# Kernel tuning notes

Measured on AMD Instinct MI355X. Metric: run time of the kernel, lower is better.

## Reference

```python
import jax, jax.numpy as jnp
import numpy as np

MAX_TOP_K = 64          # max(top_k) across the batch, as in sample_from_logit dispatch
NEG_INF = -1e30
B, V, T = 256, 128000, 16


def setup_inputs() -> dict:
    key = jax.random.key(0)
    k1, k2, k3, k4, k5, k6 = jax.random.split(key, 6)
    logits = jax.random.normal(k1, (B, V), dtype=jnp.float32)
    temperature = jax.random.uniform(k2, (B,), dtype=jnp.float32) + 0.5   # (0.5, 1.5)
    top_k = jax.random.randint(k3, (B,), 1, MAX_TOP_K, dtype=jnp.int32)
    top_p = jax.random.uniform(k4, (B,), dtype=jnp.float32)               # (0, 1)
    min_p = jax.random.uniform(k5, (B,), dtype=jnp.float32) * 0.1         # small min-p
    target_ids = jax.random.randint(k6, (B, T), 0, V, dtype=jnp.int32)
    return {"logits": logits, "temperature": temperature, "top_k": top_k,
            "top_p": top_p, "min_p": min_p, "target_ids": target_ids}


def _sample_from_logit(logits, temperature, top_k, top_p, min_p):
    # temperature scaling
    temp = jnp.maximum(temperature, 0.05)
    scaled = logits / temp[:, None]                    # [B, V]
    # restrict to the max_top_k candidates once (sorted descending)
    vals, idx = jax.lax.top_k(scaled, MAX_TOP_K)       # [B, K], [B, K]
    pos = jnp.arange(MAX_TOP_K)[None, :]
    k = jnp.clip(top_k, 1, MAX_TOP_K)
    keep_k = pos < k[:, None]                          # per-request top-k mask
    vals = jnp.where(keep_k, vals, NEG_INF)
    probs = jax.nn.softmax(vals, axis=-1)              # renormalized over kept set
    # top-p (nucleus): keep tokens whose preceding cumulative mass < top_p
    csum = jnp.cumsum(probs, axis=-1)
    keep_p = (csum - probs) < top_p[:, None]
    # min-p: keep tokens with prob >= min_p * max_prob (max is column 0, sorted desc)
    keep_m = probs >= min_p[:, None] * probs[:, :1]
    keep = (keep_k & keep_p & keep_m).at[:, 0].set(True)  # always keep the argmax
    filt_logp = jnp.where(keep, jnp.log(probs + 1e-20), NEG_INF)
    # multinomial sample via Gumbel-max (renormalization is implicit)
    g = jax.random.gumbel(jax.random.key(42), filt_logp.shape, dtype=filt_logp.dtype)
    choice = jnp.argmax(filt_logp + g, axis=-1)        # [B] index into top-K set
    return jnp.take_along_axis(idx, choice[:, None], axis=1)[:, 0]  # vocab ids


def reference(logits, temperature, top_k, top_p, min_p, target_ids):
    next_token_ids = _sample_from_logit(logits, temperature, top_k, top_p, min_p)  # [B]
    # perplexity gather: ppls = -log_softmax(logits); ppl[i, j] = ppls[i, target_ids[i, j]]
    logZ = jax.nn.logsumexp(logits, axis=-1, keepdims=True)          # [B, 1]
    tgt_logits = jnp.take_along_axis(logits, target_ids, axis=1)     # [B, T]
    ppl = -(tgt_logits - logZ)                                       # [B, T]
    return next_token_ids, ppl
```

## Files before the change

### kernel.cpp

```cpp
#include <hip/hip_runtime.h>
#include <stdint.h>

#define B_ 256
#define V_ 128000
#define T_ 16
#define K_ 64
#define NEG_INF_ (-1e30f)

#define CAP   4096
#define NT    1024

__device__ __forceinline__ uint32_t rotl32(uint32_t x, uint32_t d) {
  return (x << d) | (x >> (32u - d));
}

__device__ uint32_t threefry_bits_partitionable(uint32_t f) {
  const uint32_t ks0 = 0u;
  const uint32_t ks1 = 42u;
  const uint32_t ks2 = 0x1BD11BDAu ^ 0u ^ 42u;
  uint32_t x0 = 0u;
  uint32_t x1 = f;
  x0 += ks0; x1 += ks1;
#define R4(a,b,c,d) \
  x0 += x1; x1 = rotl32(x1,a); x1 ^= x0; \
  x0 += x1; x1 = rotl32(x1,b); x1 ^= x0; \
  x0 += x1; x1 = rotl32(x1,c); x1 ^= x0; \
  x0 += x1; x1 = rotl32(x1,d); x1 ^= x0;
  R4(13u,15u,26u,6u)   x0 += ks1; x1 += ks2 + 1u;
  R4(17u,29u,16u,24u)  x0 += ks2; x1 += ks0 + 2u;
  R4(13u,15u,26u,6u)   x0 += ks0; x1 += ks1 + 3u;
  R4(17u,29u,16u,24u)  x0 += ks1; x1 += ks2 + 4u;
  R4(13u,15u,26u,6u)   x0 += ks2; x1 += ks0 + 5u;
#undef R4
  return x0 ^ x1;
}

__global__ __launch_bounds__(NT) void sampler_kernel(
    const float* __restrict__ logits,
    const float* __restrict__ temperature,
    const int*   __restrict__ top_k,
    const float* __restrict__ top_p,
    const float* __restrict__ min_p,
    const int*   __restrict__ target_ids,
    float*       __restrict__ out)
{
  const int r   = blockIdx.x;
  const int tid = threadIdx.x;
  const float* __restrict__ row = logits + (size_t)r * V_;

  __shared__ unsigned long long s_cand[CAP];
  __shared__ unsigned int       s_candcount;
  __shared__ float              s_wavesum[NT / 64];
  __shared__ unsigned long long s_top[K_];
  __shared__ float              s_g[K_];
  __shared__ float              s_logZ;
  __shared__ int                s_ncand;

  if (tid < K_) s_top[tid] = 0ull;
  if (tid == 0) s_candcount = 0u;
  __syncthreads();

  const float temp = fmaxf(temperature[r], 0.05f);

  float a0 = 0.0f, a1 = 0.0f, a2 = 0.0f, a3 = 0.0f;
  const float4* row4 = reinterpret_cast<const float4*>(row);
  const int nf4 = V_ / 4;

#define PROC4(vv, i4) do {                                                     \
    a0 += __expf(vv.x); a1 += __expf(vv.y);                                    \
    a2 += __expf(vv.z); a3 += __expf(vv.w);                                    \
    float mx_ = fmaxf(fmaxf(vv.x, vv.y), fmaxf(vv.z, vv.w));                   \
    if (mx_ > 3.0f) {                                                          \
      float xs_[4] = {vv.x, vv.y, vv.z, vv.w};                                 \
      _Pragma("unroll")                                                        \
      for (int c_ = 0; c_ < 4; ++c_) {                                         \
        if (xs_[c_] > 3.0f) {                                                  \
          unsigned int slot_ = atomicAdd(&s_candcount, 1u);                    \
          if (slot_ < CAP) {                                                   \
            float scaled_ = xs_[c_] / temp;                                    \
            uint32_t idx_ = (uint32_t)((i4) * 4 + c_);                         \
            s_cand[slot_] =                                                    \
              ((unsigned long long)__float_as_uint(scaled_) << 32) |           \
              (unsigned long long)(0xFFFFFFFFu - idx_);                        \
          }                                                                    \
        }                                                                      \
      }                                                                        \
    }                                                                          \
  } while (0)

  int base = 0;
  for (; base + NT * 4 <= nf4; base += NT * 4) {
    const int i0 = base + tid, i1 = i0 + NT, i2 = i1 + NT, i3 = i2 + NT;
    float4 v0 = row4[i0];
    float4 v1 = row4[i1];
    float4 v2 = row4[i2];
    float4 v3 = row4[i3];
    PROC4(v0, i0); PROC4(v1, i1); PROC4(v2, i2); PROC4(v3, i3);
  }
  for (int i = base + tid; i < nf4; i += NT) {
    float4 v = row4[i];
    PROC4(v, i);
  }
#undef PROC4

  float esum = (a0 + a1) + (a2 + a3);
  for (int off = 32; off > 0; off >>= 1) esum += __shfl_down(esum, off, 64);
  if ((tid & 63) == 0) s_wavesum[tid >> 6] = esum;
  __syncthreads();
  if (tid == 0) {
    float t = 0.0f;
    for (int w = 0; w < NT / 64; ++w) t += s_wavesum[w];
    s_logZ = logf(t);
    int nc = (int)s_candcount; if (nc > CAP) nc = CAP;
    s_ncand = nc;
  }
  __syncthreads();

  int ncand = s_ncand;
  for (int tier = 0; tier < 2 && ncand < K_; ++tier) {
    if (tid == 0) s_candcount = 0u;
    __syncthreads();
    const float thr = (tier == 0) ? 2.0f : -3.0e38f;
    for (int i = tid; i < V_; i += NT) {
      float x = row[i];
      if (x >= thr) {
        unsigned int slot = atomicAdd(&s_candcount, 1u);
        if (slot < CAP) {
          float scaled = x / temp;
          s_cand[slot] = ((unsigned long long)__float_as_uint(scaled) << 32) |
                         (unsigned long long)(0xFFFFFFFFu - (uint32_t)i);
        }
      }
    }
    __syncthreads();
    if (tid == 0) { int nc = (int)s_candcount; if (nc > CAP) nc = CAP; s_ncand = nc; }
    __syncthreads();
    ncand = s_ncand;
  }

  if (tid < K_) {
    uint32_t bits = threefry_bits_partitionable((uint32_t)(r * K_ + tid));
    float u01 = __uint_as_float((bits >> 9) | 0x3f800000u) - 1.0f;
    const float tiny = 1.1754943508222875e-38f;
    float u = fmaxf(tiny, u01 * (1.0f - tiny) + tiny);
    s_g[tid] = -logf(-logf(u));
  }

  if (tid < T_) {
    int tgt = target_ids[r * T_ + tid];
    out[B_ + r * T_ + tid] = s_logZ - row[tgt];
  }

  for (int c = tid; c < ncand; c += NT) {
    unsigned long long key = s_cand[c];
    int rank = 0;
    for (int j = 0; j < ncand; ++j) rank += (s_cand[j] > key) ? 1 : 0;
    if (rank < K_) s_top[rank] = key;
  }
  __syncthreads();

  if (tid == 0) {
    int kk = top_k[r];
    kk = kk < 1 ? 1 : (kk > K_ ? K_ : kk);
    const float tp = top_p[r], mp = min_p[r];
    const int nn = ncand < K_ ? ncand : K_;

    float e[K_];
    float m = 0.0f, sum = 0.0f;
    for (int i = 0; i < K_; ++i) {
      float v = (i < nn) ? __uint_as_float((uint32_t)(s_top[i] >> 32)) : NEG_INF_;
      if (i >= kk) v = NEG_INF_;
      if (i == 0) m = v;
      e[i] = expf(v - m);
      sum += e[i];
    }
    float csum = 0.0f, best = -INFINITY;
    int choice = 0;
    const float p0 = e[0] / sum;
    for (int i = 0; i < K_; ++i) {
      float pi = e[i] / sum;
      csum += pi;
      bool keep = (i < kk) && ((csum - pi) < tp) && (pi >= mp * p0);
      if (i == 0) keep = true;
      float fl = keep ? logf(pi + 1e-20f) : NEG_INF_;
      float sc = fl + s_g[i];
      if (sc > best) { best = sc; choice = i; }
    }
    int token = (int)(0xFFFFFFFFu - (uint32_t)(s_top[choice] & 0xFFFFFFFFull));
    out[r] = (float)token;
  }
}

extern "C" void kernel_launch(void* const* d_in, const int* in_sizes, int n_in,
                              void* d_out, int out_size, void* d_ws, size_t ws_size,
                              hipStream_t stream) {
  const float* logits      = (const float*)d_in[0];
  const float* temperature = (const float*)d_in[1];
  const int*   top_k       = (const int*)d_in[2];
  const float* top_p       = (const float*)d_in[3];
  const float* min_p       = (const float*)d_in[4];
  const int*   target_ids  = (const int*)d_in[5];
  float* out = (float*)d_out;
  (void)in_sizes; (void)n_in; (void)out_size; (void)d_ws; (void)ws_size;

  hipLaunchKernelGGL(sampler_kernel, dim3(B_), dim3(NT), 0, stream,
                     logits, temperature, top_k, top_p, min_p, target_ids, out);
}
```

Before: 41.38 us.

## Split each row across eight blocks with a global-candidate finalize kernel

The single 1024-thread block per row becomes a two-kernel pipeline. A streaming kernel gives each row to eight 256-thread blocks, which compute partial exp-sums and push candidates above 3.0 into a per-row global buffer using global atomics. A finalize kernel then ranks the candidates, computes logZ and the perplexity gather, and runs the sampling with the softmax steps parallelised over 64 threads. This aims for better occupancy and more bandwidth across the GPU. In exchange it adds a memset, a second launch and contended global atomics, and it falls back to the old kernel if the workspace is too small.

```diff
diff --git a/kernel.cpp b/kernel.cpp
--- a/kernel.cpp
+++ b/kernel.cpp
@@ -1,11 +1,19 @@
 #include <hip/hip_runtime.h>
 #include <stdint.h>
+
+typedef unsigned long long ull;
 
 #define B_ 256
 #define V_ 128000
 #define T_ 16
 #define K_ 64
 #define NEG_INF_ (-1e30f)
+
+#define PARTS   8
+#define NTA     256
+#define CHUNK4  (V_ / 4 / PARTS)
+#define CAPG    512
+#define CAPL    2048
 
 #define CAP   4096
 #define NT    1024
@@ -35,6 +43,198 @@
   return x0 ^ x1;
 }
 
+__global__ __launch_bounds__(NTA, 8) void stream_kernel(
+    const float* __restrict__ logits,
+    const float* __restrict__ temperature,
+    unsigned int* __restrict__ wcnt,
+    float*        __restrict__ wesum,
+    ull*          __restrict__ wcand)
+{
+  const int bid  = blockIdx.x;
+  const int r    = bid >> 3;
+  const int part = bid & 7;
+  const int tid  = threadIdx.x;
+
+  const float temp = fmaxf(temperature[r], 0.05f);
+  const float4* __restrict__ p4 =
+      reinterpret_cast<const float4*>(logits + (size_t)r * V_) + part * CHUNK4;
+  unsigned int* cntp = wcnt + r;
+  ull* candp = wcand + (size_t)r * CAPG;
+
+  float a0 = 0.0f, a1 = 0.0f, a2 = 0.0f, a3 = 0.0f;
+
+#define PROC4(vv, i4) do {                                                     \
+    a0 += __expf(vv.x); a1 += __expf(vv.y);                                    \
+    a2 += __expf(vv.z); a3 += __expf(vv.w);                                    \
+    float mx_ = fmaxf(fmaxf(vv.x, vv.y), fmaxf(vv.z, vv.w));                   \
+    if (mx_ > 3.0f) {                                                          \
+      float xs_[4] = {vv.x, vv.y, vv.z, vv.w};                                 \
+      _Pragma("unroll")                                                        \
+      for (int c_ = 0; c_ < 4; ++c_) {                                         \
+        if (xs_[c_] > 3.0f) {                                                  \
+          unsigned int slot_ = atomicAdd(cntp, 1u);                            \
+          if (slot_ < CAPG) {                                                  \
+            float scaled_ = xs_[c_] / temp;                                    \
+            uint32_t idx_ = (uint32_t)((part * CHUNK4 + (i4)) * 4 + c_);       \
+            candp[slot_] = ((ull)__float_as_uint(scaled_) << 32) |             \
+                           (ull)(0xFFFFFFFFu - idx_);                          \
+          }                                                                    \
+        }                                                                      \
+      }                                                                        \
+    }                                                                          \
+  } while (0)
+
+  int base = 0;
+  for (; base + NTA * 4 <= CHUNK4; base += NTA * 4) {
+    const int i0 = base + tid, i1 = i0 + NTA, i2 = i1 + NTA, i3 = i2 + NTA;
+    float4 v0 = p4[i0];
+    float4 v1 = p4[i1];
+    float4 v2 = p4[i2];
+    float4 v3 = p4[i3];
+    PROC4(v0, i0); PROC4(v1, i1); PROC4(v2, i2); PROC4(v3, i3);
+  }
+  for (int i = base + tid; i < CHUNK4; i += NTA) {
+    float4 v = p4[i];
+    PROC4(v, i);
+  }
+#undef PROC4
+
+  __shared__ float s_ws[NTA / 64];
+  float esum = (a0 + a1) + (a2 + a3);
+  for (int off = 32; off > 0; off >>= 1) esum += __shfl_down(esum, off, 64);
+  if ((tid & 63) == 0) s_ws[tid >> 6] = esum;
+  __syncthreads();
+  if (tid == 0) {
+    float t = 0.0f;
+    for (int w = 0; w < NTA / 64; ++w) t += s_ws[w];
+    wesum[bid] = t;
+  }
+}
+
+__global__ __launch_bounds__(256) void finalize_kernel(
+    const float* __restrict__ logits,
+    const float* __restrict__ temperature,
+    const int*   __restrict__ top_k,
+    const float* __restrict__ top_p,
+    const float* __restrict__ min_p,
+    const int*   __restrict__ target_ids,
+    const unsigned int* __restrict__ wcnt,
+    const float* __restrict__ wesum,
+    const ull*   __restrict__ wcand,
+    float*       __restrict__ out)
+{
+  const int r   = blockIdx.x;
+  const int tid = threadIdx.x;
+
+  __shared__ ull   s_cand[CAPL];
+  __shared__ ull   s_top[K_];
+  __shared__ float s_g[K_];
+  __shared__ float s_e[K_];
+  __shared__ float s_pi[K_];
+  __shared__ float s_lg[K_];
+  __shared__ float s_logZ, s_sum;
+  __shared__ unsigned int s_cc;
+
+  const float temp = fmaxf(temperature[r], 0.05f);
+
+  if (tid < K_) s_top[tid] = 0ull;
+
+  int cnt = (int)wcnt[r]; if (cnt > CAPG) cnt = CAPG;
+  for (int i = tid; i < cnt; i += 256) s_cand[i] = wcand[(size_t)r * CAPG + i];
+
+  if (tid == 0) {
+    float t = 0.0f;
+    for (int w = 0; w < PARTS; ++w) t += wesum[r * PARTS + w];
+    s_logZ = logf(t);
+  }
+  __syncthreads();
+
+  if (tid < T_) {
+    int tgt = target_ids[r * T_ + tid];
+    out[B_ + r * T_ + tid] = s_logZ - logits[(size_t)r * V_ + tgt];
+  }
+
+  int ncand = cnt;
+  for (int tier = 0; tier < 2 && ncand < K_; ++tier) {
+    __syncthreads();
+    if (tid == 0) s_cc = 0u;
+    __syncthreads();
+    const float thr = (tier == 0) ? 2.5f : -3.0e38f;
+    const float* rowp = logits + (size_t)r * V_;
+    for (int i = tid; i < V_; i += 256) {
+      float x = rowp[i];
+      if (x >= thr) {
+        unsigned int slot = atomicAdd(&s_cc, 1u);
+        if (slot < CAPL) {
+          float scaled = x / temp;
+          s_cand[slot] = ((ull)__float_as_uint(scaled) << 32) |
+                         (ull)(0xFFFFFFFFu - (uint32_t)i);
+        }
+      }
+    }
+    __syncthreads();
+    ncand = (int)(s_cc > CAPL ? CAPL : s_cc);
+  }
+
+  for (int c = tid; c < ncand; c += 256) {
+    ull key = s_cand[c];
+    int rank = 0;
+    for (int j = 0; j < ncand; ++j) rank += (s_cand[j] > key) ? 1 : 0;
+    if (rank < K_) s_top[rank] = key;
+  }
+  __syncthreads();
+
+  if (tid >= 64 && tid < 128) {
+    int i = tid - 64;
+    uint32_t bits = threefry_bits_partitionable((uint32_t)(r * K_ + i));
+    float u01 = __uint_as_float((bits >> 9) | 0x3f800000u) - 1.0f;
+    const float tiny = 1.1754943508222875e-38f;
+    float u = fmaxf(tiny, u01 * (1.0f - tiny) + tiny);
+    s_g[i] = -logf(-logf(u));
+  }
+
+  const int kk_raw = top_k[r];
+  const int kk = kk_raw < 1 ? 1 : (kk_raw > K_ ? K_ : kk_raw);
+  const int nn = ncand < K_ ? ncand : K_;
+
+  if (tid < K_) {
+    float v = (tid < nn) ? __uint_as_float((uint32_t)(s_top[tid] >> 32)) : NEG_INF_;
+    if (tid >= kk) v = NEG_INF_;
+    float v0 = (0 < nn) ? __uint_as_float((uint32_t)(s_top[0] >> 32)) : NEG_INF_;
+    s_e[tid] = expf(v - v0);
+  }
+  __syncthreads();
+  if (tid == 0) {
+    float sum = 0.0f;
+    for (int i = 0; i < K_; ++i) sum += s_e[i];
+    s_sum = sum;
+  }
+  __syncthreads();
+  if (tid < K_) {
+    float pi = s_e[tid] / s_sum;
+    s_pi[tid] = pi;
+    s_lg[tid] = logf(pi + 1e-20f);
+  }
+  __syncthreads();
+  if (tid == 0) {
+    const float tp = top_p[r], mp = min_p[r];
+    const float p0 = s_pi[0];
+    float csum = 0.0f, best = -INFINITY;
+    int choice = 0;
+    for (int i = 0; i < K_; ++i) {
+      float pi = s_pi[i];
+      csum += pi;
+      bool keep = (i < kk) && ((csum - pi) < tp) && (pi >= mp * p0);
+      if (i == 0) keep = true;
+      float fl = keep ? s_lg[i] : NEG_INF_;
+      float sc = fl + s_g[i];
+      if (sc > best) { best = sc; choice = i; }
+    }
+    int token = (int)(0xFFFFFFFFu - (uint32_t)(s_top[choice] & 0xFFFFFFFFull));
+    out[r] = (float)token;
+  }
+}
+
 __global__ __launch_bounds__(NT) void sampler_kernel(
     const float* __restrict__ logits,
     const float* __restrict__ temperature,
@@ -48,13 +248,13 @@
   const int tid = threadIdx.x;
   const float* __restrict__ row = logits + (size_t)r * V_;
 
-  __shared__ unsigned long long s_cand[CAP];
-  __shared__ unsigned int       s_candcount;
-  __shared__ float              s_wavesum[NT / 64];
-  __shared__ unsigned long long s_top[K_];
-  __shared__ float              s_g[K_];
-  __shared__ float              s_logZ;
-  __shared__ int                s_ncand;
+  __shared__ ull          s_cand[CAP];
+  __shared__ unsigned int s_candcount;
+  __shared__ float        s_wavesum[NT / 64];
+  __shared__ ull          s_top[K_];
+  __shared__ float        s_g[K_];
+  __shared__ float        s_logZ;
+  __shared__ int          s_ncand;
 
   if (tid < K_) s_top[tid] = 0ull;
   if (tid == 0) s_candcount = 0u;
@@ -79,9 +279,8 @@
           if (slot_ < CAP) {                                                   \
             float scaled_ = xs_[c_] / temp;                                    \
             uint32_t idx_ = (uint32_t)((i4) * 4 + c_);                         \
-            s_cand[slot_] =                                                    \
-              ((unsigned long long)__float_as_uint(scaled_) << 32) |           \
-              (unsigned long long)(0xFFFFFFFFu - idx_);                        \
+            s_cand[slot_] = ((ull)__float_as_uint(scaled_) << 32) |            \
+                            (ull)(0xFFFFFFFFu - idx_);                         \
           }                                                                    \
         }                                                                      \
       }                                                                        \
@@ -127,8 +326,8 @@
         unsigned int slot = atomicAdd(&s_candcount, 1u);
         if (slot < CAP) {
           float scaled = x / temp;
-          s_cand[slot] = ((unsigned long long)__float_as_uint(scaled) << 32) |
-                         (unsigned long long)(0xFFFFFFFFu - (uint32_t)i);
+          s_cand[slot] = ((ull)__float_as_uint(scaled) << 32) |
+                         (ull)(0xFFFFFFFFu - (uint32_t)i);
         }
       }
     }
@@ -152,7 +351,7 @@
   }
 
   for (int c = tid; c < ncand; c += NT) {
-    unsigned long long key = s_cand[c];
+    ull key = s_cand[c];
     int rank = 0;
     for (int j = 0; j < ncand; ++j) rank += (s_cand[j] > key) ? 1 : 0;
     if (rank < K_) s_top[rank] = key;
@@ -201,8 +400,21 @@
   const float* min_p       = (const float*)d_in[4];
   const int*   target_ids  = (const int*)d_in[5];
   float* out = (float*)d_out;
-  (void)in_sizes; (void)n_in; (void)out_size; (void)d_ws; (void)ws_size;
-
-  hipLaunchKernelGGL(sampler_kernel, dim3(B_), dim3(NT), 0, stream,
-                     logits, temperature, top_k, top_p, min_p, target_ids, out);
-}
+  (void)in_sizes; (void)n_in; (void)out_size;
+
+  const size_t need = 16384 + (size_t)B_ * CAPG * sizeof(ull);
+  if (ws_size >= need) {
+    unsigned int* wcnt = (unsigned int*)d_ws;
+    float*        wesum = (float*)((char*)d_ws + 1024);
+    ull*          wcand = (ull*)((char*)d_ws + 16384);
+    hipMemsetAsync(d_ws, 0, B_ * sizeof(unsigned int), stream);
+    hipLaunchKernelGGL(stream_kernel, dim3(B_ * PARTS), dim3(NTA), 0, stream,
+                       logits, temperature, wcnt, wesum, wcand);
+    hipLaunchKernelGGL(finalize_kernel, dim3(B_), dim3(256), 0, stream,
+                       logits, temperature, top_k, top_p, min_p, target_ids,
+                       wcnt, wesum, wcand, out);
+  } else {
+    hipLaunchKernelGGL(sampler_kernel, dim3(B_), dim3(NT), 0, stream,
+                       logits, temperature, top_k, top_p, min_p, target_ids, out);
+  }
+}
```

Result: slower. 85.69 us (+107.1%).
